# Kernel optimization log

Measured on AMD Instinct MI355X. Metric: run time of the kernel, lower is better.

Reference implementation:

```python
import jax, jax.numpy as jnp
import numpy as np

NHID = 1024
NTOKEN = 10000
T, B = 128, 32
INITRANGE = 0.04
# DARTS recurrent genotype: (activation, predecessor-state index)
GENO = (("sigmoid", 0), ("relu", 1), ("relu", 1), ("identity", 1),
        ("tanh", 2), ("sigmoid", 5), ("tanh", 3), ("relu", 5))
CONCAT = tuple(range(1, 9))
ACT = {"sigmoid": jax.nn.sigmoid, "relu": jax.nn.relu,
       "tanh": jnp.tanh, "identity": lambda x: x}


def setup_inputs() -> dict:
    key = jax.random.key(0)
    ks = jax.random.split(key, 4)
    u = lambda k, shape: jax.random.uniform(k, shape, jnp.float32, -INITRANGE, INITRANGE)
    return {
        "tokens": jax.random.randint(ks[0], (T, B), 0, NTOKEN),
        "h0": jnp.zeros((B, NHID), jnp.float32),
        "enc_W": u(ks[1], (NTOKEN, NHID)),            # tied encoder/decoder weight
        "W0": u(ks[2], (2 * NHID, 2 * NHID)),          # (ninp+nhid, 2*nhid)
        "Ws": u(ks[3], (len(GENO), NHID, 2 * NHID)),   # one matrix per genotype edge
        "dec_b": jnp.zeros((NTOKEN,), jnp.float32),
    }


def _cell(x, h_prev, W0, Ws):
    # init state: c0,h0 from cat(x, h_prev) @ W0
    xh = jnp.concatenate([x, h_prev], axis=-1)           # (B, 2*nhid)
    c0, h0 = jnp.split(xh @ W0, 2, axis=-1)
    s = h_prev + jax.nn.sigmoid(c0) * (jnp.tanh(h0) - h_prev)
    states = [s]
    for i, (name, pred) in enumerate(GENO):
        sp = states[pred]
        c, h = jnp.split(sp @ Ws[i], 2, axis=-1)
        states.append(sp + jax.nn.sigmoid(c) * (ACT[name](h) - sp))
    # output = mean over concat states
    return sum(states[i] for i in CONCAT) / float(len(CONCAT))


def reference(tokens, h0, enc_W, W0, Ws, dec_b):
    emb = enc_W[tokens]                                  # (T, B, ninp)

    def step(h, x):
        h_new = _cell(x, h, W0, Ws)
        return h_new, h_new

    h_last, hiddens = jax.lax.scan(step, h0, emb)        # hiddens: (T, B, nhid)
    logits = hiddens @ enc_W.T + dec_b                   # tied decoder (T, B, ntoken)
    log_prob = jax.nn.log_softmax(logits, axis=-1)
    return log_prob, h_last[None]                        # ((T,B,V), (1,B,nhid))
```

## Files before the change

### kernel.cpp

```cpp
#include <hip/hip_runtime.h>
#include <cmath>

#define NHID 1024
#define NTOK 10000
#define TT 128
#define BB 32
#define BN (BB*NHID)
#define WMAT (2048*1024)
#define FSTRIDE 16

typedef __attribute__((ext_vector_type(8))) short s8v;
typedef __attribute__((ext_vector_type(4))) float f4v;

#define MFMA(a,b,c) __builtin_amdgcn_mfma_f32_16x16x32_bf16(a,b,c,0,0,0)

__device__ __forceinline__ float sigf(float x){ return 1.f/(1.f+__expf(-x)); }
__device__ __forceinline__ float actf(int a, float h){
  switch(a){ case 0: return sigf(h); case 1: return fmaxf(h,0.f);
             case 2: return tanhf(h); default: return h; }
}
__device__ __forceinline__ unsigned short f2bf(float x){
  union { float f; unsigned u; } v; v.f = x;
  unsigned r = v.u + 0x7fffu + ((v.u >> 16) & 1u);
  return (unsigned short)(r >> 16);
}

__device__ __forceinline__ void ld_f2(const float* p, float& x0, float& x1){
  unsigned long long u = __hip_atomic_load((const unsigned long long*)p,
                         __ATOMIC_RELAXED, __HIP_MEMORY_SCOPE_AGENT);
  union { unsigned long long u; float f[2]; } v; v.u = u;
  x0 = v.f[0]; x1 = v.f[1];
}

__device__ __forceinline__ void coh_ld16(const unsigned short* pa, const unsigned short* pb,
                                         s8v A[8], s8v B[8]){
  asm volatile(
    "global_load_dwordx4 %0, %16, off sc0 sc1\n\t"
    "global_load_dwordx4 %1, %16, off offset:64 sc0 sc1\n\t"
    "global_load_dwordx4 %2, %16, off offset:128 sc0 sc1\n\t"
    "global_load_dwordx4 %3, %16, off offset:192 sc0 sc1\n\t"
    "global_load_dwordx4 %4, %16, off offset:256 sc0 sc1\n\t"
    "global_load_dwordx4 %5, %16, off offset:320 sc0 sc1\n\t"
    "global_load_dwordx4 %6, %16, off offset:384 sc0 sc1\n\t"
    "global_load_dwordx4 %7, %16, off offset:448 sc0 sc1\n\t"
    "global_load_dwordx4 %8, %17, off sc0 sc1\n\t"
    "global_load_dwordx4 %9, %17, off offset:64 sc0 sc1\n\t"
    "global_load_dwordx4 %10, %17, off offset:128 sc0 sc1\n\t"
    "global_load_dwordx4 %11, %17, off offset:192 sc0 sc1\n\t"
    "global_load_dwordx4 %12, %17, off offset:256 sc0 sc1\n\t"
    "global_load_dwordx4 %13, %17, off offset:320 sc0 sc1\n\t"
    "global_load_dwordx4 %14, %17, off offset:384 sc0 sc1\n\t"
    "global_load_dwordx4 %15, %17, off offset:448 sc0 sc1\n\t"
    "s_waitcnt vmcnt(0)"
    : "=&v"(A[0]),"=&v"(A[1]),"=&v"(A[2]),"=&v"(A[3]),
      "=&v"(A[4]),"=&v"(A[5]),"=&v"(A[6]),"=&v"(A[7]),
      "=&v"(B[0]),"=&v"(B[1]),"=&v"(B[2]),"=&v"(B[3]),
      "=&v"(B[4]),"=&v"(B[5]),"=&v"(B[6]),"=&v"(B[7])
    : "v"(pa), "v"(pb)
    : "memory");
}

__device__ __forceinline__ void st_wt32(void* p, unsigned x){
  asm volatile("global_store_dword %0, %1, off sc0 sc1" :: "v"(p), "v"(x) : "memory");
}
__device__ __forceinline__ void st_wt64(void* p, unsigned long long x){
  asm volatile("global_store_dwordx2 %0, %1, off sc0 sc1" :: "v"(p), "v"(x) : "memory");
}
__device__ __forceinline__ unsigned long long packf2(float a, float b){
  union { float f[2]; unsigned long long u; } v; v.f[0]=a; v.f[1]=b; return v.u;
}


__global__ __launch_bounds__(256) void k_transpose_cvt(
    const float* __restrict__ W0, const float* __restrict__ Ws,
    unsigned short* __restrict__ dstAll)
{
  int z = blockIdx.z;
  const float* src = (z==0) ? W0 : (z==1) ? (W0 + (size_t)1024*2048)
                                          : (Ws + (size_t)(z-2)*1024*2048);
  unsigned short* dst = dstAll + (size_t)z*WMAT;
  __shared__ float tile[32][33];
  int n0 = blockIdx.x*32;
  int k0 = blockIdx.y*32;
  int tx = threadIdx.x & 31, ty = threadIdx.x >> 5;
  #pragma unroll
  for (int i=0;i<4;i++){
    int k = k0 + ty + i*8;
    tile[ty + i*8][tx] = src[(size_t)k*2048 + n0 + tx];
  }
  __syncthreads();
  #pragma unroll
  for (int i=0;i<4;i++){
    int n = n0 + ty + i*8;
    dst[(size_t)n*1024 + k0 + tx] = f2bf(tile[tx][ty + i*8]);
  }
}

__global__ void k_cvt(const float* __restrict__ src, unsigned short* __restrict__ dst, int n){
  int i = blockIdx.x*blockDim.x + threadIdx.x;
  int stride = gridDim.x*blockDim.x;
  for (; i < n; i += stride) dst[i] = f2bf(src[i]);
}

__global__ void k_zero(unsigned* __restrict__ p, int n){
  int i = blockIdx.x*blockDim.x + threadIdx.x;
  if (i < n) p[i] = 0u;
}


__device__ __forceinline__ void poll1(const unsigned* F, int idx, unsigned tgt){
  const unsigned* f = F + (size_t)idx*FSTRIDE;
  while (__hip_atomic_load(f, __ATOMIC_RELAXED, __HIP_MEMORY_SCOPE_AGENT) < tgt)
    __builtin_amdgcn_s_sleep(2);
}
__device__ __forceinline__ void signal(unsigned* F, int s, int tile, unsigned val){
  asm volatile("s_waitcnt vmcnt(0)" ::: "memory");
  __syncthreads();
  if (threadIdx.x == 0)
    st_wt32((void*)(F + (size_t)((s<<6)+tile)*FSTRIDE), val);
}

struct B8 { s8v c[8]; s8v h[8]; };

__device__ __forceinline__ void load_b8(const unsigned short* __restrict__ Wt,
                                        int z, int j0, int r, int kb, int q, B8& B){
  const unsigned short* wz = Wt + (size_t)z*WMAT;
  const s8v* bc = (const s8v*)(wz + (size_t)(j0+r)*1024 + kb);
  const s8v* bh = (const s8v*)(wz + (size_t)(1024+j0+r)*1024 + kb);
  #pragma unroll
  for (int i=0;i<8;i++){ B.c[i]=bc[q+4*i]; B.h[i]=bh[q+4*i]; }
}

__device__ __forceinline__ void do_edge_reg(
    const B8& B, float* __restrict__ st_f,
    unsigned short* __restrict__ st_bf, float* __restrict__ red,
    unsigned* __restrict__ F, int pred, int outs, int act,
    int j0, int tile, unsigned tgt, int wave, int q, int r, int tid)
{
  int lane = tid & 63;
  if (lane < 17){
    int idx = (pred<<6) + ((lane<16) ? (wave*16 + lane) : tile);
    poll1(F, idx, tgt);
  }
  int row = tid>>3, col = (tid&7)*2;
  size_t off = (size_t)row*NHID + j0 + col;
  float sp0, sp1;
  ld_f2(st_f + (size_t)pred*BN + off, sp0, sp1);
  const unsigned short* spb = st_bf + (size_t)pred*BN;
  int kb = wave*256;
  s8v a0[8], a1[8];
  coh_ld16(spb + (size_t)r*NHID + kb + q*8,
           spb + (size_t)(16+r)*NHID + kb + q*8, a0, a1);
  f4v zz = {0.f,0.f,0.f,0.f};
  f4v aC0=zz,aC1=zz,aH0=zz,aH1=zz;
  #pragma unroll
  for (int i=0;i<8;i++){
    aC0=MFMA(a0[i],B.c[i],aC0); aC1=MFMA(a1[i],B.c[i],aC1);
    aH0=MFMA(a0[i],B.h[i],aH0); aH1=MFMA(a1[i],B.h[i],aH1);
  }
  #pragma unroll
  for (int i=0;i<4;i++){
    red[((wave*4+0)*32 + q*4+i)*16 + r]    = aC0[i];
    red[((wave*4+0)*32 + 16+q*4+i)*16 + r] = aC1[i];
    red[((wave*4+1)*32 + q*4+i)*16 + r]    = aH0[i];
    red[((wave*4+1)*32 + 16+q*4+i)*16 + r] = aH1[i];
  }
  __syncthreads();
  float cs0=0,cs1=0,hs0=0,hs1=0;
  #pragma unroll
  for (int w2=0; w2<4; w2++){
    cs0 += red[((w2*4+0)*32+row)*16+col];
    cs1 += red[((w2*4+0)*32+row)*16+col+1];
    hs0 += red[((w2*4+1)*32+row)*16+col];
    hs1 += red[((w2*4+1)*32+row)*16+col+1];
  }
  float v0 = sp0 + sigf(cs0)*(actf(act,hs0) - sp0);
  float v1 = sp1 + sigf(cs1)*(actf(act,hs1) - sp1);
  st_wt64(&st_f[(size_t)outs*BN+off], packf2(v0, v1));
  unsigned pk = (unsigned)f2bf(v0) | ((unsigned)f2bf(v1)<<16);
  st_wt32((unsigned*)(st_bf + (size_t)outs*BN + off), pk);
  signal(F, outs, tile, tgt);
}

__global__ __launch_bounds__(256, 1) void k_recur(
    const int* __restrict__ tok, const float* __restrict__ h0f,
    const unsigned short* __restrict__ encb,
    const unsigned short* __restrict__ Wt,
    const unsigned short* __restrict__ h0b,
    float* __restrict__ st_f, unsigned short* __restrict__ st_bf,
    float* __restrict__ h_f, unsigned short* __restrict__ h_bf,
    unsigned short* __restrict__ hid_bf, unsigned* __restrict__ F)
{
  __shared__ float red[4*4*32*16];
  int wg = blockIdx.x, grp = wg >> 6, tile = wg & 63;
  int tid = threadIdx.x, wave = tid>>6, lane = tid&63, q = lane>>4, r = lane&15;
  int j0 = tile * 16;

  if (grp == 0) {
    B8 BX; load_b8(Wt, 0, j0, r, wave*256, q, BX);
    B8 BH; load_b8(Wt, 1, j0, r, wave*256, q, BH);
    B8 B3; load_b8(Wt, 5, j0, r, wave*256, q, B3);

    for (int t = 0; t < TT; ++t) {
      unsigned tgt = t+1;
      s8v xa0[8], xa1[8];
      {
        int kb = wave * 256;
        const s8v* e0p = (const s8v*)(encb + (size_t)tok[t*BB + r]*NHID + kb);
        const s8v* e1p = (const s8v*)(encb + (size_t)tok[t*BB + 16 + r]*NHID + kb);
        #pragma unroll
        for (int i=0;i<8;i++){ xa0[i]=e0p[q+4*i]; xa1[i]=e1p[q+4*i]; }
      }
      if (t && lane < 17){
        int idx = (8<<6) + ((lane<16) ? (wave*16 + lane) : tile);
        poll1(F, idx, t);
      }
      int row = tid>>3, col = (tid&7)*2;
      size_t off = (size_t)row*NHID + j0 + col;
      const float* hfb = t ? h_f : h0f;
      float hp0, hp1; ld_f2(hfb + off, hp0, hp1);
      const unsigned short* hb = t ? h_bf : h0b;
      int kb = wave*256;
      s8v ha0[8], ha1[8];
      coh_ld16(hb + (size_t)r*NHID + kb + q*8,
               hb + (size_t)(16+r)*NHID + kb + q*8, ha0, ha1);
      f4v zz = {0.f,0.f,0.f,0.f};
      f4v aC0=zz,aC1=zz,aH0=zz,aH1=zz;
      #pragma unroll
      for (int i=0;i<8;i++){
        aC0=MFMA(xa0[i],BX.c[i],aC0); aC1=MFMA(xa1[i],BX.c[i],aC1);
        aH0=MFMA(xa0[i],BX.h[i],aH0); aH1=MFMA(xa1[i],BX.h[i],aH1);
      }
      #pragma unroll
      for (int i=0;i<8;i++){
        aC0=MFMA(ha0[i],BH.c[i],aC0); aC1=MFMA(ha1[i],BH.c[i],aC1);
        aH0=MFMA(ha0[i],BH.h[i],aH0); aH1=MFMA(ha1[i],BH.h[i],aH1);
      }
      #pragma unroll
      for (int i=0;i<4;i++){
        red[((wave*4+0)*32 + q*4+i)*16 + r]    = aC0[i];
        red[((wave*4+0)*32 + 16+q*4+i)*16 + r] = aC1[i];
        red[((wave*4+1)*32 + q*4+i)*16 + r]    = aH0[i];
        red[((wave*4+1)*32 + 16+q*4+i)*16 + r] = aH1[i];
      }
      __syncthreads();
      float cs0=0,cs1=0,hs0=0,hs1=0;
      #pragma unroll
      for (int w2=0; w2<4; w2++){
        cs0 += red[((w2*4+0)*32+row)*16+col];
        cs1 += red[((w2*4+0)*32+row)*16+col+1];
        hs0 += red[((w2*4+1)*32+row)*16+col];
        hs1 += red[((w2*4+1)*32+row)*16+col+1];
      }
      float v0 = hp0 + sigf(cs0)*(tanhf(hs0)-hp0);
      float v1 = hp1 + sigf(cs1)*(tanhf(hs1)-hp1);
      st_wt64(&st_f[off], packf2(v0, v1));
      unsigned pk = (unsigned)f2bf(v0) | ((unsigned)f2bf(v1)<<16);
      st_wt32((unsigned*)(st_bf + off), pk);
      signal(F, 0, tile, tgt);
      do_edge_reg(B3, st_f, st_bf, red, F, 1, 4, 3, j0, tile, tgt, wave, q, r, tid);
    }
  } else if (grp == 1) {
    B8 B0; load_b8(Wt, 2, j0, r, wave*256, q, B0);
    B8 B4; load_b8(Wt, 6, j0, r, wave*256, q, B4);
    for (int t = 0; t < TT; ++t) {
      unsigned tgt = t+1;
      do_edge_reg(B0, st_f, st_bf, red, F, 0, 1, 0, j0, tile, tgt, wave, q, r, tid);
      do_edge_reg(B4, st_f, st_bf, red, F, 2, 5, 2, j0, tile, tgt, wave, q, r, tid);
    }
  } else if (grp == 2) {
    B8 B1; load_b8(Wt, 3, j0, r, wave*256, q, B1);
    B8 B6; load_b8(Wt, 8, j0, r, wave*256, q, B6);
    for (int t = 0; t < TT; ++t) {
      unsigned tgt = t+1;
      do_edge_reg(B1, st_f, st_bf, red, F, 1, 2, 1, j0, tile, tgt, wave, q, r, tid);
      do_edge_reg(B6, st_f, st_bf, red, F, 3, 7, 2, j0, tile, tgt, wave, q, r, tid);
    }
  } else {
    B8 B2; load_b8(Wt, 4, j0, r, wave*256, q, B2);
    B8 B5; load_b8(Wt, 7, j0, r, wave*256, q, B5);
    B8 B7; load_b8(Wt, 9, j0, r, wave*256, q, B7);
    for (int t = 0; t < TT; ++t) {
      unsigned tgt = t+1;
      do_edge_reg(B2, st_f, st_bf, red, F, 1, 3, 1, j0, tile, tgt, wave, q, r, tid);
      if (lane < 19){
        int idx = (lane<16) ? ((5<<6) + wave*16 + lane)
                : (lane==16) ? ((4<<6)+tile)
                : (lane==17) ? ((5<<6)+tile) : ((7<<6)+tile);
        poll1(F, idx, tgt);
      }
      {
        int row = tid>>3, col = (tid&7)*2;
        size_t off = (size_t)row*NHID + j0 + col;
        float s1a,s1b,s2a,s2b,s3a,s3b,s4a,s4b,s5a,s5b,s7a,s7b;
        ld_f2(st_f + (size_t)1*BN + off, s1a, s1b);
        ld_f2(st_f + (size_t)2*BN + off, s2a, s2b);
        ld_f2(st_f + (size_t)3*BN + off, s3a, s3b);
        ld_f2(st_f + (size_t)4*BN + off, s4a, s4b);
        ld_f2(st_f + (size_t)5*BN + off, s5a, s5b);
        ld_f2(st_f + (size_t)7*BN + off, s7a, s7b);
        const unsigned short* spb = st_bf + (size_t)5*BN;
        int kb = wave*256;
        s8v a0[8], a1[8];
        coh_ld16(spb + (size_t)r*NHID + kb + q*8,
                 spb + (size_t)(16+r)*NHID + kb + q*8, a0, a1);
        f4v zz = {0.f,0.f,0.f,0.f};
        f4v c50=zz,c51=zz,h50=zz,h51=zz,c70=zz,c71=zz,h70=zz,h71=zz;
        #pragma unroll
        for (int i=0;i<8;i++){
          c50=MFMA(a0[i],B5.c[i],c50); c51=MFMA(a1[i],B5.c[i],c51);
          h50=MFMA(a0[i],B5.h[i],h50); h51=MFMA(a1[i],B5.h[i],h51);
          c70=MFMA(a0[i],B7.c[i],c70); c71=MFMA(a1[i],B7.c[i],c71);
          h70=MFMA(a0[i],B7.h[i],h70); h71=MFMA(a1[i],B7.h[i],h71);
        }
        #pragma unroll
        for (int i=0;i<4;i++){
          red[((wave*4+0)*32 + q*4+i)*16 + r]    = c50[i];
          red[((wave*4+0)*32 + 16+q*4+i)*16 + r] = c51[i];
          red[((wave*4+1)*32 + q*4+i)*16 + r]    = h50[i];
          red[((wave*4+1)*32 + 16+q*4+i)*16 + r] = h51[i];
          red[((wave*4+2)*32 + q*4+i)*16 + r]    = c70[i];
          red[((wave*4+2)*32 + 16+q*4+i)*16 + r] = c71[i];
          red[((wave*4+3)*32 + q*4+i)*16 + r]    = h70[i];
          red[((wave*4+3)*32 + 16+q*4+i)*16 + r] = h71[i];
        }
        __syncthreads();
        float a5c[2]={0,0}, a5h[2]={0,0}, a7c[2]={0,0}, a7h[2]={0,0};
        #pragma unroll
        for (int w2=0; w2<4; w2++){
          #pragma unroll
          for (int u=0; u<2; u++){
            a5c[u] += red[((w2*4+0)*32+row)*16+col+u];
            a5h[u] += red[((w2*4+1)*32+row)*16+col+u];
            a7c[u] += red[((w2*4+2)*32+row)*16+col+u];
            a7h[u] += red[((w2*4+3)*32+row)*16+col+u];
          }
        }
        float s5v[2] = {s5a, s5b};
        float o1[2] = {s1a, s1b}, o2[2] = {s2a, s2b}, o3[2] = {s3a, s3b};
        float o4[2] = {s4a, s4b}, o7[2] = {s7a, s7b};
        float hv[2];
        #pragma unroll
        for (int u=0; u<2; u++){
          float s5j = s5v[u];
          float s6 = s5j + sigf(a5c[u])*(sigf(a5h[u]) - s5j);
          float s8 = s5j + sigf(a7c[u])*(fmaxf(a7h[u],0.f) - s5j);
          float sum = o1[u] + o2[u] + o3[u] + o4[u]
                    + s5j + s6 + o7[u] + s8;
          hv[u] = 0.125f * sum;
        }
        st_wt64(&h_f[off], packf2(hv[0], hv[1]));
        unsigned pk = (unsigned)f2bf(hv[0]) | ((unsigned)f2bf(hv[1])<<16);
        st_wt32((unsigned*)(h_bf + off), pk);
        *(unsigned*)(hid_bf + (size_t)t*BN + off) = pk;
        signal(F, 8, tile, tgt);
      }
    }
  }
}


__global__ __launch_bounds__(256) void k_decoder(
    const unsigned short* __restrict__ Hb, const unsigned short* __restrict__ Wb,
    float* __restrict__ out)
{
  int L = blockIdx.x;
  int xcd = L & 7, i = L >> 3;
  int band = i / 320;
  int r2 = i % 320;
  int bnIdx = r2 >> 4, bmi = r2 & 15;
  int bn_t = xcd + 8*bnIdx;
  if (bn_t >= 157) return;
  int bm_t = band*16 + bmi;
  int wave = threadIdx.x >> 6, lane = threadIdx.x & 63;
  int q = lane >> 4, r = lane & 15;
  int bm = bm_t*64 + (wave>>1)*32;
  int bn = bn_t*64 + (wave&1)*32;
  f4v z = {0.f,0.f,0.f,0.f};
  f4v acc00=z, acc01=z, acc10=z, acc11=z;
  const s8v* a0p = (const s8v*)(Hb + (size_t)(bm + r)*NHID);
  const s8v* a1p = (const s8v*)(Hb + (size_t)(bm + 16 + r)*NHID);
  int n0 = bn + r, n1 = bn + 16 + r;
  const s8v* b0p = (const s8v*)(Wb + (size_t)(n0 < NTOK ? n0 : 0)*NHID);
  const s8v* b1p = (const s8v*)(Wb + (size_t)(n1 < NTOK ? n1 : 0)*NHID);
  #pragma unroll 4
  for (int v = q; v < 128; v += 4) {
    s8v a0 = a0p[v], a1 = a1p[v], b0 = b0p[v], b1 = b1p[v];
    acc00 = MFMA(a0, b0, acc00); acc10 = MFMA(a1, b0, acc10);
    acc01 = MFMA(a0, b1, acc01); acc11 = MFMA(a1, b1, acc11);
  }
  #pragma unroll
  for (int ni=0; ni<2; ni++){
    int col = bn + ni*16 + r;
    if (col >= NTOK) continue;
    #pragma unroll
    for (int mi=0; mi<2; mi++){
      f4v a = (mi==0) ? (ni==0 ? acc00 : acc01) : (ni==0 ? acc10 : acc11);
      #pragma unroll
      for (int t4=0; t4<4; t4++){
        int row = bm + mi*16 + q*4 + t4;
        out[(size_t)row*NTOK + col] = a[t4];
      }
    }
  }
}

__global__ __launch_bounds__(256) void k_logsoftmax(
    float* __restrict__ logits, const float* __restrict__ bias)
{
  size_t row = blockIdx.x;
  float* p = logits + row * NTOK;
  float v[40];
  float mx = -1e30f;
  #pragma unroll
  for (int i=0;i<40;i++){
    int c = threadIdx.x + (i<<8);
    float x = (c < NTOK) ? (p[c] + bias[c]) : -1e30f;
    v[i] = x; mx = fmaxf(mx, x);
  }
  #pragma unroll
  for (int off=32; off>0; off>>=1) mx = fmaxf(mx, __shfl_down(mx, off));
  __shared__ float red[4], red2[4];
  int wv = threadIdx.x>>6, ln = threadIdx.x&63;
  if (ln==0) red[wv] = mx;
  __syncthreads();
  mx = fmaxf(fmaxf(red[0],red[1]), fmaxf(red[2],red[3]));
  float s = 0.f;
  #pragma unroll
  for (int i=0;i<40;i++) s += __expf(v[i] - mx);
  #pragma unroll
  for (int off=32; off>0; off>>=1) s += __shfl_down(s, off);
  if (ln==0) red2[wv] = s;
  __syncthreads();
  s = red2[0]+red2[1]+red2[2]+red2[3];
  float lse = mx + __logf(s);
  #pragma unroll
  for (int i=0;i<40;i++){
    int c = threadIdx.x + (i<<8);
    if (c < NTOK) p[c] = v[i] - lse;
  }
}

__global__ void k_copy(const float* __restrict__ src, float* __restrict__ dst, int n){
  int i = blockIdx.x*blockDim.x + threadIdx.x;
  if (i < n) dst[i] = src[i];
}


extern "C" void kernel_launch(void* const* d_in, const int* in_sizes, int n_in,
                              void* d_out, int out_size, void* d_ws, size_t ws_size,
                              hipStream_t stream) {
  const int*   tok  = (const int*)d_in[0];
  const float* h0   = (const float*)d_in[1];
  const float* encw = (const float*)d_in[2];
  const float* W0   = (const float*)d_in[3];
  const float* Ws   = (const float*)d_in[4];
  const float* decb = (const float*)d_in[5];
  float* out = (float*)d_out;

  char* w = (char*)d_ws;
  unsigned short* Wt      = (unsigned short*)w; w += (size_t)10*WMAT*2;
  unsigned short* encw_bf = (unsigned short*)w; w += (size_t)NTOK*NHID*2;
  unsigned short* h0_bf   = (unsigned short*)w; w += (size_t)BN*2;
  unsigned short* hid_bf  = (unsigned short*)w; w += (size_t)TT*BN*2;
  float*          st_f    = (float*)w;          w += (size_t)9*BN*4;
  unsigned short* st_bf   = (unsigned short*)w; w += (size_t)9*BN*2;
  float*          h_f     = (float*)w;          w += (size_t)BN*4;
  unsigned short* h_bf    = (unsigned short*)w; w += (size_t)BN*2;
  unsigned*       flags   = (unsigned*)w;       w += (size_t)576*FSTRIDE*4;

  k_zero<<<36, 256, 0, stream>>>(flags, 576*FSTRIDE);
  k_transpose_cvt<<<dim3(64,32,10), 256, 0, stream>>>(W0, Ws, Wt);
  k_cvt<<<4096, 256, 0, stream>>>(encw, encw_bf, NTOK*NHID);
  k_cvt<<<128, 256, 0, stream>>>(h0, h0_bf, BN);

  k_recur<<<256, 256, 0, stream>>>(tok, h0, encw_bf, Wt, h0_bf,
                                   st_f, st_bf, h_f, h_bf, hid_bf, flags);

  k_decoder<<<10240, 256, 0, stream>>>(hid_bf, encw_bf, out);
  k_logsoftmax<<<TT*BB, 256, 0, stream>>>(out, decb);
  k_copy<<<128, 256, 0, stream>>>(h_f, out + (size_t)TT*BB*NTOK, BN);
}
```

Before: 3.553 ms.

## Rebalance recurrent cell edges across workgroups and widen decoder tiles

```diff
diff --git a/kernel.cpp b/kernel.cpp
--- a/kernel.cpp
+++ b/kernel.cpp
@@ -23,6 +23,9 @@
   union { float f; unsigned u; } v; v.f = x;
   unsigned r = v.u + 0x7fffu + ((v.u >> 16) & 1u);
   return (unsigned short)(r >> 16);
+}
+__device__ __forceinline__ unsigned pkbf(float a, float b){
+  return (unsigned)f2bf(a) | ((unsigned)f2bf(b)<<16);
 }
 
 __device__ __forceinline__ void ld_f2(const float* p, float& x0, float& x1){
@@ -111,7 +114,7 @@
 __device__ __forceinline__ void poll1(const unsigned* F, int idx, unsigned tgt){
   const unsigned* f = F + (size_t)idx*FSTRIDE;
   while (__hip_atomic_load(f, __ATOMIC_RELAXED, __HIP_MEMORY_SCOPE_AGENT) < tgt)
-    __builtin_amdgcn_s_sleep(2);
+    __builtin_amdgcn_s_sleep(1);
 }
 __device__ __forceinline__ void signal(unsigned* F, int s, int tile, unsigned val){
   asm volatile("s_waitcnt vmcnt(0)" ::: "memory");
@@ -120,7 +123,8 @@
     st_wt32((void*)(F + (size_t)((s<<6)+tile)*FSTRIDE), val);
 }
 
-struct B8 { s8v c[8]; s8v h[8]; };
+struct B8  { s8v c[8]; s8v h[8]; };
+struct B16v{ s8v c0[8], c1[8], h0[8], h1[8]; };
 
 __device__ __forceinline__ void load_b8(const unsigned short* __restrict__ Wt,
                                         int z, int j0, int r, int kb, int q, B8& B){
@@ -130,16 +134,28 @@
   #pragma unroll
   for (int i=0;i<8;i++){ B.c[i]=bc[q+4*i]; B.h[i]=bh[q+4*i]; }
 }
-
-__device__ __forceinline__ void do_edge_reg(
+__device__ __forceinline__ void load_b16(const unsigned short* __restrict__ Wt,
+                                         int z, int j0, int r, int kb, int q, B16v& B){
+  const unsigned short* wz = Wt + (size_t)z*WMAT;
+  const s8v* c0 = (const s8v*)(wz + (size_t)(j0+r)*1024 + kb);
+  const s8v* c1 = (const s8v*)(wz + (size_t)(j0+16+r)*1024 + kb);
+  const s8v* h0 = (const s8v*)(wz + (size_t)(1024+j0+r)*1024 + kb);
+  const s8v* h1 = (const s8v*)(wz + (size_t)(1024+j0+16+r)*1024 + kb);
+  #pragma unroll
+  for (int i=0;i<8;i++){ B.c0[i]=c0[q+4*i]; B.c1[i]=c1[q+4*i];
+                         B.h0[i]=h0[q+4*i]; B.h1[i]=h1[q+4*i]; }
+}
+
+template<int NPRED>
+__device__ __forceinline__ void do_edge16(
     const B8& B, float* __restrict__ st_f,
     unsigned short* __restrict__ st_bf, float* __restrict__ red,
     unsigned* __restrict__ F, int pred, int outs, int act,
-    int j0, int tile, unsigned tgt, int wave, int q, int r, int tid)
+    int j0, int tile16, int ownIdx, unsigned tgt, int wave, int q, int r, int tid)
 {
   int lane = tid & 63;
-  if (lane < 17){
-    int idx = (pred<<6) + ((lane<16) ? (wave*16 + lane) : tile);
+  if (lane < NPRED+1){
+    int idx = (pred<<6) + ((lane<NPRED) ? (wave*NPRED + lane) : ownIdx);
     poll1(F, idx, tgt);
   }
   int row = tid>>3, col = (tid&7)*2;
@@ -177,9 +193,71 @@
   float v0 = sp0 + sigf(cs0)*(actf(act,hs0) - sp0);
   float v1 = sp1 + sigf(cs1)*(actf(act,hs1) - sp1);
   st_wt64(&st_f[(size_t)outs*BN+off], packf2(v0, v1));
-  unsigned pk = (unsigned)f2bf(v0) | ((unsigned)f2bf(v1)<<16);
-  st_wt32((unsigned*)(st_bf + (size_t)outs*BN + off), pk);
-  signal(F, outs, tile, tgt);
+  st_wt32((unsigned*)(st_bf + (size_t)outs*BN + off), pkbf(v0, v1));
+  signal(F, outs, tile16, tgt);
+}
+
+template<int NPRED, int NOWN>
+__device__ __forceinline__ void do_edge32(
+    const B16v& B, float* __restrict__ st_f,
+    unsigned short* __restrict__ st_bf, float* __restrict__ red,
+    unsigned* __restrict__ F, int pred, int outs, int act,
+    int j0, int tile32, int ownBase, unsigned tgt, int wave, int q, int r, int tid)
+{
+  int lane = tid & 63;
+  if (lane < NPRED+NOWN){
+    int idx = (pred<<6) + ((lane<NPRED) ? (wave*NPRED + lane) : (ownBase + lane - NPRED));
+    poll1(F, idx, tgt);
+  }
+  int row = tid>>3, col = (tid&7)*2;
+  size_t off  = (size_t)row*NHID + j0 + col;
+  size_t off2 = off + 16;
+  float sA0,sA1,sB0,sB1;
+  ld_f2(st_f + (size_t)pred*BN + off,  sA0, sA1);
+  ld_f2(st_f + (size_t)pred*BN + off2, sB0, sB1);
+  const unsigned short* spb = st_bf + (size_t)pred*BN;
+  int kb = wave*256;
+  s8v a0[8], a1[8];
+  coh_ld16(spb + (size_t)r*NHID + kb + q*8,
+           spb + (size_t)(16+r)*NHID + kb + q*8, a0, a1);
+  f4v zz = {0.f,0.f,0.f,0.f};
+  f4v C00=zz,C01=zz,C10=zz,C11=zz,H00=zz,H01=zz,H10=zz,H11=zz;
+  #pragma unroll
+  for (int i=0;i<8;i++){
+    C00=MFMA(a0[i],B.c0[i],C00); C10=MFMA(a1[i],B.c0[i],C10);
+    C01=MFMA(a0[i],B.c1[i],C01); C11=MFMA(a1[i],B.c1[i],C11);
+    H00=MFMA(a0[i],B.h0[i],H00); H10=MFMA(a1[i],B.h0[i],H10);
+    H01=MFMA(a0[i],B.h1[i],H01); H11=MFMA(a1[i],B.h1[i],H11);
+  }
+  #pragma unroll
+  for (int i=0;i<4;i++){
+    red[((wave*4+0)*32 + q*4+i)*16 + r]    = C00[i];
+    red[((wave*4+0)*32 + 16+q*4+i)*16 + r] = C10[i];
+    red[((wave*4+1)*32 + q*4+i)*16 + r]    = C01[i];
+    red[((wave*4+1)*32 + 16+q*4+i)*16 + r] = C11[i];
+    red[((wave*4+2)*32 + q*4+i)*16 + r]    = H00[i];
+    red[((wave*4+2)*32 + 16+q*4+i)*16 + r] = H10[i];
+    red[((wave*4+3)*32 + q*4+i)*16 + r]    = H01[i];
+    red[((wave*4+3)*32 + 16+q*4+i)*16 + r] = H11[i];
+  }
+  __syncthreads();
+  float c00=0,c01=0,c10=0,c11=0,h00=0,h01=0,h10=0,h11=0;
+  #pragma unroll
+  for (int w2=0; w2<4; w2++){
+    c00 += red[((w2*4+0)*32+row)*16+col];  c01 += red[((w2*4+0)*32+row)*16+col+1];
+    c10 += red[((w2*4+1)*32+row)*16+col];  c11 += red[((w2*4+1)*32+row)*16+col+1];
+    h00 += red[((w2*4+2)*32+row)*16+col];  h01 += red[((w2*4+2)*32+row)*16+col+1];
+    h10 += red[((w2*4+3)*32+row)*16+col];  h11 += red[((w2*4+3)*32+row)*16+col+1];
+  }
+  float v00 = sA0 + sigf(c00)*(actf(act,h00)-sA0);
+  float v01 = sA1 + sigf(c01)*(actf(act,h01)-sA1);
+  float v10 = sB0 + sigf(c10)*(actf(act,h10)-sB0);
+  float v11 = sB1 + sigf(c11)*(actf(act,h11)-sB1);
+  st_wt64(&st_f[(size_t)outs*BN+off],  packf2(v00,v01));
+  st_wt64(&st_f[(size_t)outs*BN+off2], packf2(v10,v11));
+  st_wt32((unsigned*)(st_bf+(size_t)outs*BN+off),  pkbf(v00,v01));
+  st_wt32((unsigned*)(st_bf+(size_t)outs*BN+off2), pkbf(v10,v11));
+  signal(F, outs, tile32, tgt);
 }
 
 __global__ __launch_bounds__(256, 1) void k_recur(
@@ -192,14 +270,15 @@
     unsigned short* __restrict__ hid_bf, unsigned* __restrict__ F)
 {
   __shared__ float red[4*4*32*16];
-  int wg = blockIdx.x, grp = wg >> 6, tile = wg & 63;
+  int wg = blockIdx.x;
   int tid = threadIdx.x, wave = tid>>6, lane = tid&63, q = lane>>4, r = lane&15;
-  int j0 = tile * 16;
-
-  if (grp == 0) {
+
+  if (wg < 64) {
+    int tile16 = wg, j0 = tile16*16;
     B8 BX; load_b8(Wt, 0, j0, r, wave*256, q, BX);
     B8 BH; load_b8(Wt, 1, j0, r, wave*256, q, BH);
     B8 B3; load_b8(Wt, 5, j0, r, wave*256, q, B3);
+    B8 B6; load_b8(Wt, 8, j0, r, wave*256, q, B6);
 
     for (int t = 0; t < TT; ++t) {
       unsigned tgt = t+1;
@@ -212,7 +291,7 @@
         for (int i=0;i<8;i++){ xa0[i]=e0p[q+4*i]; xa1[i]=e1p[q+4*i]; }
       }
       if (t && lane < 17){
-        int idx = (8<<6) + ((lane<16) ? (wave*16 + lane) : tile);
+        int idx = (8<<6) + ((lane<16) ? (wave*16 + lane) : tile16);
         poll1(F, idx, t);
       }
       int row = tid>>3, col = (tid&7)*2;
@@ -255,107 +334,111 @@
       float v0 = hp0 + sigf(cs0)*(tanhf(hs0)-hp0);
       float v1 = hp1 + sigf(cs1)*(tanhf(hs1)-hp1);
       st_wt64(&st_f[off], packf2(v0, v1));
-      unsigned pk = (unsigned)f2bf(v0) | ((unsigned)f2bf(v1)<<16);
-      st_wt32((unsigned*)(st_bf + off), pk);
-      signal(F, 0, tile, tgt);
-      do_edge_reg(B3, st_f, st_bf, red, F, 1, 4, 3, j0, tile, tgt, wave, q, r, tid);
+      st_wt32((unsigned*)(st_bf + off), pkbf(v0, v1));
+      signal(F, 0, tile16, tgt);
+      do_edge16<8>(B3, st_f, st_bf, red, F, 1, 4, 3, j0, tile16, tile16>>1, tgt, wave, q, r, tid);
+      do_edge16<8>(B6, st_f, st_bf, red, F, 3, 7, 2, j0, tile16, tile16>>1, tgt, wave, q, r, tid);
     }
-  } else if (grp == 1) {
-    B8 B0; load_b8(Wt, 2, j0, r, wave*256, q, B0);
-    B8 B4; load_b8(Wt, 6, j0, r, wave*256, q, B4);
-    for (int t = 0; t < TT; ++t) {
-      unsigned tgt = t+1;
-      do_edge_reg(B0, st_f, st_bf, red, F, 0, 1, 0, j0, tile, tgt, wave, q, r, tid);
-      do_edge_reg(B4, st_f, st_bf, red, F, 2, 5, 2, j0, tile, tgt, wave, q, r, tid);
-    }
-  } else if (grp == 2) {
-    B8 B1; load_b8(Wt, 3, j0, r, wave*256, q, B1);
-    B8 B6; load_b8(Wt, 8, j0, r, wave*256, q, B6);
-    for (int t = 0; t < TT; ++t) {
-      unsigned tgt = t+1;
-      do_edge_reg(B1, st_f, st_bf, red, F, 1, 2, 1, j0, tile, tgt, wave, q, r, tid);
-      do_edge_reg(B6, st_f, st_bf, red, F, 3, 7, 2, j0, tile, tgt, wave, q, r, tid);
-    }
-  } else {
-    B8 B2; load_b8(Wt, 4, j0, r, wave*256, q, B2);
+  } else if (wg < 128) {
+    int tile16 = wg - 64, j0 = tile16*16;
     B8 B5; load_b8(Wt, 7, j0, r, wave*256, q, B5);
     B8 B7; load_b8(Wt, 9, j0, r, wave*256, q, B7);
     for (int t = 0; t < TT; ++t) {
       unsigned tgt = t+1;
-      do_edge_reg(B2, st_f, st_bf, red, F, 1, 3, 1, j0, tile, tgt, wave, q, r, tid);
-      if (lane < 19){
-        int idx = (lane<16) ? ((5<<6) + wave*16 + lane)
-                : (lane==16) ? ((4<<6)+tile)
-                : (lane==17) ? ((5<<6)+tile) : ((7<<6)+tile);
+      if (lane < 11){
+        int idx = (lane<8) ? ((5<<6) + wave*8 + lane)
+                : (lane==8) ? ((4<<6) + tile16)
+                : (lane==9) ? ((5<<6) + (tile16>>1)) : ((7<<6) + tile16);
         poll1(F, idx, tgt);
       }
-      {
-        int row = tid>>3, col = (tid&7)*2;
-        size_t off = (size_t)row*NHID + j0 + col;
-        float s1a,s1b,s2a,s2b,s3a,s3b,s4a,s4b,s5a,s5b,s7a,s7b;
-        ld_f2(st_f + (size_t)1*BN + off, s1a, s1b);
-        ld_f2(st_f + (size_t)2*BN + off, s2a, s2b);
-        ld_f2(st_f + (size_t)3*BN + off, s3a, s3b);
-        ld_f2(st_f + (size_t)4*BN + off, s4a, s4b);
-        ld_f2(st_f + (size_t)5*BN + off, s5a, s5b);
-        ld_f2(st_f + (size_t)7*BN + off, s7a, s7b);
-        const unsigned short* spb = st_bf + (size_t)5*BN;
-        int kb = wave*256;
-        s8v a0[8], a1[8];
-        coh_ld16(spb + (size_t)r*NHID + kb + q*8,
-                 spb + (size_t)(16+r)*NHID + kb + q*8, a0, a1);
-        f4v zz = {0.f,0.f,0.f,0.f};
-        f4v c50=zz,c51=zz,h50=zz,h51=zz,c70=zz,c71=zz,h70=zz,h71=zz;
-        #pragma unroll
-        for (int i=0;i<8;i++){
-          c50=MFMA(a0[i],B5.c[i],c50); c51=MFMA(a1[i],B5.c[i],c51);
-          h50=MFMA(a0[i],B5.h[i],h50); h51=MFMA(a1[i],B5.h[i],h51);
-          c70=MFMA(a0[i],B7.c[i],c70); c71=MFMA(a1[i],B7.c[i],c71);
-          h70=MFMA(a0[i],B7.h[i],h70); h71=MFMA(a1[i],B7.h[i],h71);
-        }
-        #pragma unroll
-        for (int i=0;i<4;i++){
-          red[((wave*4+0)*32 + q*4+i)*16 + r]    = c50[i];
-          red[((wave*4+0)*32 + 16+q*4+i)*16 + r] = c51[i];
-          red[((wave*4+1)*32 + q*4+i)*16 + r]    = h50[i];
-          red[((wave*4+1)*32 + 16+q*4+i)*16 + r] = h51[i];
-          red[((wave*4+2)*32 + q*4+i)*16 + r]    = c70[i];
-          red[((wave*4+2)*32 + 16+q*4+i)*16 + r] = c71[i];
-          red[((wave*4+3)*32 + q*4+i)*16 + r]    = h70[i];
-          red[((wave*4+3)*32 + 16+q*4+i)*16 + r] = h71[i];
-        }
-        __syncthreads();
-        float a5c[2]={0,0}, a5h[2]={0,0}, a7c[2]={0,0}, a7h[2]={0,0};
-        #pragma unroll
-        for (int w2=0; w2<4; w2++){
-          #pragma unroll
-          for (int u=0; u<2; u++){
-            a5c[u] += red[((w2*4+0)*32+row)*16+col+u];
-            a5h[u] += red[((w2*4+1)*32+row)*16+col+u];
-            a7c[u] += red[((w2*4+2)*32+row)*16+col+u];
-            a7h[u] += red[((w2*4+3)*32+row)*16+col+u];
-          }
-        }
-        float s5v[2] = {s5a, s5b};
-        float o1[2] = {s1a, s1b}, o2[2] = {s2a, s2b}, o3[2] = {s3a, s3b};
-        float o4[2] = {s4a, s4b}, o7[2] = {s7a, s7b};
-        float hv[2];
+      int row = tid>>3, col = (tid&7)*2;
+      size_t off = (size_t)row*NHID + j0 + col;
+      float s1a,s1b,s2a,s2b,s3a,s3b,s4a,s4b,s5a,s5b,s7a,s7b;
+      ld_f2(st_f + (size_t)1*BN + off, s1a, s1b);
+      ld_f2(st_f + (size_t)2*BN + off, s2a, s2b);
+      ld_f2(st_f + (size_t)3*BN + off, s3a, s3b);
+      ld_f2(st_f + (size_t)4*BN + off, s4a, s4b);
+      ld_f2(st_f + (size_t)5*BN + off, s5a, s5b);
+      ld_f2(st_f + (size_t)7*BN + off, s7a, s7b);
+      const unsigned short* spb = st_bf + (size_t)5*BN;
+      int kb = wave*256;
+      s8v a0[8], a1[8];
+      coh_ld16(spb + (size_t)r*NHID + kb + q*8,
+               spb + (size_t)(16+r)*NHID + kb + q*8, a0, a1);
+      f4v zz = {0.f,0.f,0.f,0.f};
+      f4v c50=zz,c51=zz,h50=zz,h51=zz,c70=zz,c71=zz,h70=zz,h71=zz;
+      #pragma unroll
+      for (int i=0;i<8;i++){
+        c50=MFMA(a0[i],B5.c[i],c50); c51=MFMA(a1[i],B5.c[i],c51);
+        h50=MFMA(a0[i],B5.h[i],h50); h51=MFMA(a1[i],B5.h[i],h51);
+      }
+      #pragma unroll
+      for (int i=0;i<8;i++){
+        c70=MFMA(a0[i],B7.c[i],c70); c71=MFMA(a1[i],B7.c[i],c71);
+        h70=MFMA(a0[i],B7.h[i],h70); h71=MFMA(a1[i],B7.h[i],h71);
+      }
+      #pragma unroll
+      for (int i=0;i<4;i++){
+        red[((wave*4+0)*32 + q*4+i)*16 + r]    = c50[i];
+        red[((wave*4+0)*32 + 16+q*4+i)*16 + r] = c51[i];
+        red[((wave*4+1)*32 + q*4+i)*16 + r]    = h50[i];
+        red[((wave*4+1)*32 + 16+q*4+i)*16 + r] = h51[i];
+        red[((wave*4+2)*32 + q*4+i)*16 + r]    = c70[i];
+        red[((wave*4+2)*32 + 16+q*4+i)*16 + r] = c71[i];
+        red[((wave*4+3)*32 + q*4+i)*16 + r]    = h70[i];
+        red[((wave*4+3)*32 + 16+q*4+i)*16 + r] = h71[i];
+      }
+      __syncthreads();
+      float a5c[2]={0,0}, a5h[2]={0,0}, a7c[2]={0,0}, a7h[2]={0,0};
+      #pragma unroll
+      for (int w2=0; w2<4; w2++){
         #pragma unroll
         for (int u=0; u<2; u++){
-          float s5j = s5v[u];
-          float s6 = s5j + sigf(a5c[u])*(sigf(a5h[u]) - s5j);
-          float s8 = s5j + sigf(a7c[u])*(fmaxf(a7h[u],0.f) - s5j);
-          float sum = o1[u] + o2[u] + o3[u] + o4[u]
-                    + s5j + s6 + o7[u] + s8;
-          hv[u] = 0.125f * sum;
+          a5c[u] += red[((w2*4+0)*32+row)*16+col+u];
+          a5h[u] += red[((w2*4+1)*32+row)*16+col+u];
+          a7c[u] += red[((w2*4+2)*32+row)*16+col+u];
+          a7h[u] += red[((w2*4+3)*32+row)*16+col+u];
         }
-        st_wt64(&h_f[off], packf2(hv[0], hv[1]));
-        unsigned pk = (unsigned)f2bf(hv[0]) | ((unsigned)f2bf(hv[1])<<16);
-        st_wt32((unsigned*)(h_bf + off), pk);
-        *(unsigned*)(hid_bf + (size_t)t*BN + off) = pk;
-        signal(F, 8, tile, tgt);
-      }
+      }
+      float s5v[2] = {s5a, s5b};
+      float o1[2] = {s1a, s1b}, o2[2] = {s2a, s2b}, o3[2] = {s3a, s3b};
+      float o4[2] = {s4a, s4b}, o7[2] = {s7a, s7b};
+      float hv[2];
+      #pragma unroll
+      for (int u=0; u<2; u++){
+        float s5j = s5v[u];
+        float s6 = s5j + sigf(a5c[u])*(sigf(a5h[u]) - s5j);
+        float s8 = s5j + sigf(a7c[u])*(fmaxf(a7h[u],0.f) - s5j);
+        float sum = o1[u] + o2[u] + o3[u] + o4[u]
+                  + s5j + s6 + o7[u] + s8;
+        hv[u] = 0.125f * sum;
+      }
+      st_wt64(&h_f[off], packf2(hv[0], hv[1]));
+      unsigned pk = pkbf(hv[0], hv[1]);
+      st_wt32((unsigned*)(h_bf + off), pk);
+      *(unsigned*)(hid_bf + (size_t)t*BN + off) = pk;
+      signal(F, 8, tile16, tgt);
     }
+  } else if (wg < 160) {
+    int tile32 = wg - 128, j0 = tile32*32;
+    B16v B; load_b16(Wt, 2, j0, r, wave*256, q, B);
+    for (int t = 0; t < TT; ++t)
+      do_edge32<16,2>(B, st_f, st_bf, red, F, 0, 1, 0, j0, tile32, 2*tile32, t+1, wave, q, r, tid);
+  } else if (wg < 192) {
+    int tile32 = wg - 160, j0 = tile32*32;
+    B16v B; load_b16(Wt, 3, j0, r, wave*256, q, B);
+    for (int t = 0; t < TT; ++t)
+      do_edge32<8,1>(B, st_f, st_bf, red, F, 1, 2, 1, j0, tile32, tile32, t+1, wave, q, r, tid);
+  } else if (wg < 224) {
+    int tile32 = wg - 192, j0 = tile32*32;
+    B16v B; load_b16(Wt, 6, j0, r, wave*256, q, B);
+    for (int t = 0; t < TT; ++t)
+      do_edge32<8,1>(B, st_f, st_bf, red, F, 2, 5, 2, j0, tile32, tile32, t+1, wave, q, r, tid);
+  } else {
+    int tile32 = wg - 224, j0 = tile32*32;
+    B16v B; load_b16(Wt, 4, j0, r, wave*256, q, B);
+    for (int t = 0; t < TT; ++t)
+      do_edge32<8,1>(B, st_f, st_bf, red, F, 1, 3, 1, j0, tile32, tile32, t+1, wave, q, r, tid);
   }
 }
 
@@ -364,43 +447,44 @@
     const unsigned short* __restrict__ Hb, const unsigned short* __restrict__ Wb,
     float* __restrict__ out)
 {
-  int L = blockIdx.x;
-  int xcd = L & 7, i = L >> 3;
-  int band = i / 320;
-  int r2 = i % 320;
-  int bnIdx = r2 >> 4, bmi = r2 & 15;
-  int bn_t = xcd + 8*bnIdx;
-  if (bn_t >= 157) return;
-  int bm_t = band*16 + bmi;
-  int wave = threadIdx.x >> 6, lane = threadIdx.x & 63;
+  int wv = threadIdx.x >> 6, lane = threadIdx.x & 63;
   int q = lane >> 4, r = lane & 15;
-  int bm = bm_t*64 + (wave>>1)*32;
-  int bn = bn_t*64 + (wave&1)*32;
-  f4v z = {0.f,0.f,0.f,0.f};
-  f4v acc00=z, acc01=z, acc10=z, acc11=z;
+  int bm = blockIdx.y*64 + (wv&1)*32;
+  int bn = blockIdx.x*128 + (wv>>1)*64;
   const s8v* a0p = (const s8v*)(Hb + (size_t)(bm + r)*NHID);
   const s8v* a1p = (const s8v*)(Hb + (size_t)(bm + 16 + r)*NHID);
-  int n0 = bn + r, n1 = bn + 16 + r;
-  const s8v* b0p = (const s8v*)(Wb + (size_t)(n0 < NTOK ? n0 : 0)*NHID);
-  const s8v* b1p = (const s8v*)(Wb + (size_t)(n1 < NTOK ? n1 : 0)*NHID);
+  const s8v* bp0; const s8v* bp1; const s8v* bp2; const s8v* bp3;
+  {
+    int c0 = bn + r,      c1 = bn + 16 + r;
+    int c2 = bn + 32 + r, c3 = bn + 48 + r;
+    bp0 = (const s8v*)(Wb + (size_t)(c0 < NTOK ? c0 : 0)*NHID);
+    bp1 = (const s8v*)(Wb + (size_t)(c1 < NTOK ? c1 : 0)*NHID);
+    bp2 = (const s8v*)(Wb + (size_t)(c2 < NTOK ? c2 : 0)*NHID);
+    bp3 = (const s8v*)(Wb + (size_t)(c3 < NTOK ? c3 : 0)*NHID);
+  }
+  f4v z = {0.f,0.f,0.f,0.f};
+  f4v acc00=z,acc01=z,acc02=z,acc03=z;
+  f4v acc10=z,acc11=z,acc12=z,acc13=z;
   #pragma unroll 4
   for (int v = q; v < 128; v += 4) {
-    s8v a0 = a0p[v], a1 = a1p[v], b0 = b0p[v], b1 = b1p[v];
+    s8v a0 = a0p[v], a1 = a1p[v];
+    s8v b0 = bp0[v], b1 = bp1[v], b2 = bp2[v], b3 = bp3[v];
     acc00 = MFMA(a0, b0, acc00); acc10 = MFMA(a1, b0, acc10);
     acc01 = MFMA(a0, b1, acc01); acc11 = MFMA(a1, b1, acc11);
-  }
-  #pragma unroll
-  for (int ni=0; ni<2; ni++){
-    int col = bn + ni*16 + r;
+    acc02 = MFMA(a0, b2, acc02); acc12 = MFMA(a1, b2, acc12);
+    acc03 = MFMA(a0, b3, acc03); acc13 = MFMA(a1, b3, acc13);
+  }
+  #pragma unroll
+  for (int n=0; n<4; n++){
+    int col = bn + n*16 + r;
     if (col >= NTOK) continue;
+    f4v am0 = (n==0)?acc00:(n==1)?acc01:(n==2)?acc02:acc03;
+    f4v am1 = (n==0)?acc10:(n==1)?acc11:(n==2)?acc12:acc13;
     #pragma unroll
-    for (int mi=0; mi<2; mi++){
-      f4v a = (mi==0) ? (ni==0 ? acc00 : acc01) : (ni==0 ? acc10 : acc11);
-      #pragma unroll
-      for (int t4=0; t4<4; t4++){
-        int row = bm + mi*16 + q*4 + t4;
-        out[(size_t)row*NTOK + col] = a[t4];
-      }
+    for (int i=0; i<4; i++){
+      int row0 = bm + q*4 + i;
+      out[(size_t)row0*NTOK + col]      = am0[i];
+      out[(size_t)(row0+16)*NTOK + col] = am1[i];
     }
   }
 }
@@ -477,7 +561,7 @@
   k_recur<<<256, 256, 0, stream>>>(tok, h0, encw_bf, Wt, h0_bf,
                                    st_f, st_bf, h_f, h_bf, hid_bf, flags);
 
-  k_decoder<<<10240, 256, 0, stream>>>(hid_bf, encw_bf, out);
+  k_decoder<<<dim3(79,64), 256, 0, stream>>>(hid_bf, encw_bf, out);
   k_logsoftmax<<<TT*BB, 256, 0, stream>>>(out, decb);
   k_copy<<<128, 256, 0, stream>>>(h_f, out + (size_t)TT*BB*NTOK, BN);
 }
```

Result: slower. 3.671 ms (+3.3%).
